# Kernel tuning notes

Hardware: AMD Instinct MI355X
Metric: run time of the kernel (lower is better)

## Reference

```python
import jax, jax.numpy as jnp
import numpy as np

N_NODES = 50000
N_EDGES = 800000
N_LABEL_EDGES = 200000
IN_CH = 256
HID = 64
OUT_CH = 64


def gcn_conv(x, W, b, edge_index, n_nodes):
    """PyG GCNConv: symmetric-normalized aggregation with self-loops.
    out[col] = sum_row norm(row,col) * (x @ W)[row] + b
    """
    xw = x @ W  # [N, out]
    loops = jnp.arange(n_nodes, dtype=edge_index.dtype)
    row = jnp.concatenate([edge_index[0], loops])  # source
    col = jnp.concatenate([edge_index[1], loops])  # target
    deg = jax.ops.segment_sum(jnp.ones_like(col, dtype=xw.dtype), col, num_segments=n_nodes)
    dis = jnp.where(deg > 0, jax.lax.rsqrt(deg), 0.0)
    norm = dis[row] * dis[col]  # [E+N]
    out = jax.ops.segment_sum(xw[row] * norm[:, None], col, num_segments=n_nodes)
    return out + b


def setup_inputs() -> dict:
    key = jax.random.key(0)
    k0, k1, k2, k3, k4 = jax.random.split(key, 5)
    x = jax.random.normal(k0, (N_NODES, IN_CH), dtype=jnp.float32)
    edge_index = jax.random.randint(k1, (2, N_EDGES), 0, N_NODES, dtype=jnp.int32)
    edge_label_index = jax.random.randint(k2, (2, N_LABEL_EDGES), 0, N_NODES, dtype=jnp.int32)
    W1 = jax.random.normal(k3, (IN_CH, HID), dtype=jnp.float32) * (1.0 / np.sqrt(IN_CH))
    b1 = jnp.zeros((HID,), dtype=jnp.float32)
    W2 = jax.random.normal(k4, (HID, OUT_CH), dtype=jnp.float32) * (1.0 / np.sqrt(HID))
    b2 = jnp.zeros((OUT_CH,), dtype=jnp.float32)
    return {"x": x, "edge_index": edge_index, "edge_label_index": edge_label_index,
            "W1": W1, "b1": b1, "W2": W2, "b2": b2}


def reference(x, edge_index, edge_label_index, W1, b1, W2, b2):
    n = x.shape[0]
    # encode: two GCNConv layers with ReLU between
    h = jax.nn.relu(gcn_conv(x, W1, b1, edge_index, n))
    z = gcn_conv(h, W2, b2, edge_index, n)
    # decode: gather node pairs, elementwise multiply, sum over features
    src, dst = edge_label_index[0], edge_label_index[1]
    return jnp.sum(z[src] * z[dst], axis=1)  # [N_LABEL_EDGES]
```

## Files before the change

### kernel.cpp

```cpp
#include <hip/hip_runtime.h>
#include <hip/hip_bf16.h>


constexpr int NC = 512;
constexpr int NBPAD = 256;
constexpr int BSHIFT = 8;

using short8 = __attribute__((ext_vector_type(8))) short;
using f32x4 = __attribute__((ext_vector_type(4))) float;

__device__ __forceinline__ unsigned short f2bf(float f) {
    unsigned u = __float_as_uint(f);
    return (unsigned short)((u + 0x7FFF + ((u >> 16) & 1)) >> 16);
}
__device__ __forceinline__ float bf2f(unsigned short h) {
    return __uint_as_float(((unsigned)h) << 16);
}
__device__ __forceinline__ float4 bf4_to_f4(ushort4 u) {
    return make_float4(bf2f(u.x), bf2f(u.y), bf2f(u.z), bf2f(u.w));
}

__global__ __launch_bounds__(256) void pack_kernel(const float* __restrict__ W1,
                                                   const float* __restrict__ W2,
                                                   unsigned short* __restrict__ Wp1,
                                                   unsigned short* __restrict__ Wp2,
                                                   int* __restrict__ bsums) {
    const int t = threadIdx.x, b = blockIdx.x;
    if (b == 0) {
        bsums[t] = 0;
    } else if (b <= 64) {
        const int idx = (b - 1) * 256 + t;
        const int k = idx >> 6, c = idx & 63;
        Wp1[((k >> 3) * 64 + c) * 8 + (k & 7)] = f2bf(W1[idx]);
    } else {
        const int idx = (b - 65) * 256 + t;
        const int k = idx >> 6, c = idx & 63;
        Wp2[((k >> 3) * 64 + c) * 8 + (k & 7)] = f2bf(W2[idx]);
    }
}

__global__ __launch_bounds__(256) void hist_kernel(const int* __restrict__ col,
                                                   int* __restrict__ histBM,
                                                   int* __restrict__ bsums, int E, int CE) {
    __shared__ int hl[NBPAD];
    const int t = threadIdx.x, c = blockIdx.x;
    hl[t] = 0;
    __syncthreads();
    const int s = c * CE, e = min(E, s + CE);
    for (int i = s + t; i < e; i += 256) atomicAdd(&hl[col[i] >> BSHIFT], 1);
    __syncthreads();
    const int v = hl[t];
    histBM[t * NC + c] = v;
    if (v) atomicAdd(&bsums[t], v);
}

__global__ __launch_bounds__(256) void rowscan_kernel(const int* __restrict__ histBM,
                                                      const int* __restrict__ bsums,
                                                      int* __restrict__ offsBM) {
    __shared__ int red[256];
    __shared__ int sc[256];
    const int t = threadIdx.x, b = blockIdx.x;
    red[t] = (t < b) ? bsums[t] : 0;
    __syncthreads();
    for (int off = 128; off > 0; off >>= 1) {
        if (t < off) red[t] += red[t + off];
        __syncthreads();
    }
    const int base = red[0];
    const int2 a = *(const int2*)&histBM[b * NC + 2 * t];
    const int a0 = a.x, a1 = a.y;
    const int ps = a0 + a1;
    sc[t] = ps;
    __syncthreads();
    for (int off = 1; off < 256; off <<= 1) {
        int u = (t >= off) ? sc[t - off] : 0;
        __syncthreads();
        sc[t] += u;
        __syncthreads();
    }
    const int excl = sc[t] - ps;
    offsBM[b * NC + 2 * t] = base + excl;
    offsBM[b * NC + 2 * t + 1] = base + excl + a0;
}

__global__ __launch_bounds__(256) void reorder_kernel(const int* __restrict__ row,
                                                      const int* __restrict__ col,
                                                      const int* __restrict__ offsBM,
                                                      int* __restrict__ part, int E, int CE) {
    __shared__ int cur[NBPAD];
    const int t = threadIdx.x, c = blockIdx.x;
    cur[t] = offsBM[t * NC + c];
    __syncthreads();
    const int s = c * CE, e = min(E, s + CE);
    for (int i = s + t; i < e; i += 256) {
        const int r = row[i], cl = col[i];
        const int p = atomicAdd(&cur[cl >> BSHIFT], 1);
        part[p] = (r << 8) | (cl & 255);
    }
}

__global__ __launch_bounds__(1024) void bucket_csr_kernel(const int* __restrict__ part,
                                                          const int* __restrict__ offsBM,
                                                          int* __restrict__ csr,
                                                          int* __restrict__ offs,
                                                          float* __restrict__ dis,
                                                          int N, int E, int nbk) {
    __shared__ int cnt[256];
    __shared__ int sc[256];
    const int t = threadIdx.x, b = blockIdx.x;
    const int base = b << BSHIFT;
    const int bstart = offsBM[b * NC];
    const int bend = (b + 1 < NBPAD) ? offsBM[(b + 1) * NC] : E;
    const int m = bend - bstart;
    if (t < 256) cnt[t] = 0;
    __syncthreads();
    for (int i = t; i < m; i += 1024) atomicAdd(&cnt[part[bstart + i] & 255], 1);
    __syncthreads();
    int v = 0;
    if (t < 256) { v = cnt[t]; sc[t] = v; }
    __syncthreads();
    for (int off = 1; off < 256; off <<= 1) {
        int u = 0;
        if (t >= off && t < 256) u = sc[t - off];
        __syncthreads();
        if (t < 256) sc[t] += u;
        __syncthreads();
    }
    if (t < 256) {
        const int excl = sc[t] - v;
        const int node = base + t;
        if (node < N) {
            offs[node] = bstart + excl;
            dis[node] = rsqrtf((float)(v + 1));
        }
        sc[t] = excl;
    }
    __syncthreads();
    for (int i = t; i < m; i += 1024) {
        const int pc = part[bstart + i];
        const int p = atomicAdd(&sc[pc & 255], 1);
        csr[bstart + p] = pc >> 8;
    }
    if (b == nbk - 1 && t == 0) offs[N] = E;
}

template <int K>
__global__ __launch_bounds__(256) void gemm_mfma(const float* __restrict__ X,
                                                 const unsigned short* __restrict__ Wp,
                                                 const float* __restrict__ rowscale,
                                                 unsigned short* __restrict__ Y, int nrows) {
    const int tid = threadIdx.x;
    const int wv = tid >> 6;
    const int lane = tid & 63;
    const int m = lane & 15;
    const int quad = lane >> 4;
    const int rowbase = blockIdx.x * 64 + wv * 16;

    int grow = rowbase + m;
    if (grow >= nrows) grow = nrows - 1;
    const float* xrow = X + (long)grow * K + quad * 8;

    f32x4 acc0 = {0.f, 0.f, 0.f, 0.f};
    f32x4 acc1 = acc0, acc2 = acc0, acc3 = acc0;

    #pragma unroll
    for (int ks = 0; ks < K / 32; ++ks) {
        const float4 a0 = *(const float4*)(xrow + ks * 32);
        const float4 a1 = *(const float4*)(xrow + ks * 32 + 4);
        short8 af;
        af[0] = (short)f2bf(a0.x); af[1] = (short)f2bf(a0.y);
        af[2] = (short)f2bf(a0.z); af[3] = (short)f2bf(a0.w);
        af[4] = (short)f2bf(a1.x); af[5] = (short)f2bf(a1.y);
        af[6] = (short)f2bf(a1.z); af[7] = (short)f2bf(a1.w);
        const unsigned short* bp = Wp + (size_t)((ks * 4 + quad) * 64) * 8;
        const short8 b0 = *(const short8*)(bp + (0 * 16 + m) * 8);
        const short8 b1 = *(const short8*)(bp + (1 * 16 + m) * 8);
        const short8 b2 = *(const short8*)(bp + (2 * 16 + m) * 8);
        const short8 b3 = *(const short8*)(bp + (3 * 16 + m) * 8);
        acc0 = __builtin_amdgcn_mfma_f32_16x16x32_bf16(af, b0, acc0, 0, 0, 0);
        acc1 = __builtin_amdgcn_mfma_f32_16x16x32_bf16(af, b1, acc1, 0, 0, 0);
        acc2 = __builtin_amdgcn_mfma_f32_16x16x32_bf16(af, b2, acc2, 0, 0, 0);
        acc3 = __builtin_amdgcn_mfma_f32_16x16x32_bf16(af, b3, acc3, 0, 0, 0);
    }

    #pragma unroll
    for (int reg = 0; reg < 4; ++reg) {
        const int orow = rowbase + quad * 4 + reg;
        if (orow < nrows) {
            const float d = rowscale[orow];
            unsigned short* yp = Y + (size_t)orow * 64 + m;
            yp[0]  = f2bf(d * acc0[reg]);
            yp[16] = f2bf(d * acc1[reg]);
            yp[32] = f2bf(d * acc2[reg]);
            yp[48] = f2bf(d * acc3[reg]);
        }
    }
}

__device__ __forceinline__ void acc8(float* a, short8 v) {
    #pragma unroll
    for (int j = 0; j < 8; ++j) a[j] += bf2f((unsigned short)v[j]);
}

__global__ __launch_bounds__(256) void agg_gemm_fused(const unsigned short* __restrict__ xs,
                                                      const int* __restrict__ csr,
                                                      const int* __restrict__ offs,
                                                      const float* __restrict__ dis,
                                                      const float* __restrict__ b1,
                                                      const unsigned short* __restrict__ Wp2,
                                                      unsigned short* __restrict__ Y, int n) {
    const int tid = threadIdx.x;
    const int wv = tid >> 6;
    const int lane = tid & 63;
    const int m = lane & 15;
    const int q = lane >> 4;
    const int rowbase = blockIdx.x * 64 + wv * 16;

    int i = rowbase + m;
    if (i >= n) i = n - 1;
    const int off_lo = q * 8;

    float alo[8], ahi[8];
    {
        const unsigned short* xrow = xs + (size_t)i * 64;
        const short8 s0 = *(const short8*)(xrow + off_lo);
        const short8 s1 = *(const short8*)(xrow + 32 + off_lo);
        #pragma unroll
        for (int j = 0; j < 8; ++j) { alo[j] = bf2f((unsigned short)s0[j]); ahi[j] = bf2f((unsigned short)s1[j]); }
    }

    const int s = offs[i];
    const int e = offs[i + 1];
    int j = s;
    int r0 = 0, r1 = 0, r2 = 0, r3 = 0;
    if (j + 3 < e) { r0 = csr[j]; r1 = csr[j + 1]; r2 = csr[j + 2]; r3 = csr[j + 3]; }
    while (j + 3 < e) {
        const int jn = j + 4;
        const int c0 = min(jn,     e - 1), c1 = min(jn + 1, e - 1);
        const int c2 = min(jn + 2, e - 1), c3 = min(jn + 3, e - 1);
        const int n0 = csr[c0], n1 = csr[c1], n2 = csr[c2], n3 = csr[c3];
        const short8 v0l = *(const short8*)(xs + (size_t)r0 * 64 + off_lo);
        const short8 v0h = *(const short8*)(xs + (size_t)r0 * 64 + 32 + off_lo);
        const short8 v1l = *(const short8*)(xs + (size_t)r1 * 64 + off_lo);
        const short8 v1h = *(const short8*)(xs + (size_t)r1 * 64 + 32 + off_lo);
        const short8 v2l = *(const short8*)(xs + (size_t)r2 * 64 + off_lo);
        const short8 v2h = *(const short8*)(xs + (size_t)r2 * 64 + 32 + off_lo);
        const short8 v3l = *(const short8*)(xs + (size_t)r3 * 64 + off_lo);
        const short8 v3h = *(const short8*)(xs + (size_t)r3 * 64 + 32 + off_lo);
        acc8(alo, v0l); acc8(ahi, v0h);
        acc8(alo, v1l); acc8(ahi, v1h);
        acc8(alo, v2l); acc8(ahi, v2h);
        acc8(alo, v3l); acc8(ahi, v3h);
        r0 = n0; r1 = n1; r2 = n2; r3 = n3;
        j = jn;
    }
    for (; j < e; ++j) {
        const int r = csr[j];
        const short8 vl = *(const short8*)(xs + (size_t)r * 64 + off_lo);
        const short8 vh = *(const short8*)(xs + (size_t)r * 64 + 32 + off_lo);
        acc8(alo, vl); acc8(ahi, vh);
    }

    const float di = dis[i];
    float bl[8], bh[8];
    *(float4*)&bl[0] = *(const float4*)(b1 + off_lo);
    *(float4*)&bl[4] = *(const float4*)(b1 + off_lo + 4);
    *(float4*)&bh[0] = *(const float4*)(b1 + 32 + off_lo);
    *(float4*)&bh[4] = *(const float4*)(b1 + 32 + off_lo + 4);
    short8 ha, hb;
    #pragma unroll
    for (int jj = 0; jj < 8; ++jj) {
        ha[jj] = (short)f2bf(fmaxf(fmaf(alo[jj], di, bl[jj]), 0.f));
        hb[jj] = (short)f2bf(fmaxf(fmaf(ahi[jj], di, bh[jj]), 0.f));
    }

    const unsigned short* bplo = Wp2 + (size_t)(q * 64) * 8;
    const unsigned short* bphi = Wp2 + (size_t)((4 + q) * 64) * 8;
    f32x4 c0 = {0.f, 0.f, 0.f, 0.f};
    f32x4 c1 = c0, c2 = c0, c3 = c0;
    const short8 w0l = *(const short8*)(bplo + (0 * 16 + m) * 8);
    const short8 w1l = *(const short8*)(bplo + (1 * 16 + m) * 8);
    const short8 w2l = *(const short8*)(bplo + (2 * 16 + m) * 8);
    const short8 w3l = *(const short8*)(bplo + (3 * 16 + m) * 8);
    const short8 w0h = *(const short8*)(bphi + (0 * 16 + m) * 8);
    const short8 w1h = *(const short8*)(bphi + (1 * 16 + m) * 8);
    const short8 w2h = *(const short8*)(bphi + (2 * 16 + m) * 8);
    const short8 w3h = *(const short8*)(bphi + (3 * 16 + m) * 8);
    c0 = __builtin_amdgcn_mfma_f32_16x16x32_bf16(ha, w0l, c0, 0, 0, 0);
    c0 = __builtin_amdgcn_mfma_f32_16x16x32_bf16(hb, w0h, c0, 0, 0, 0);
    c1 = __builtin_amdgcn_mfma_f32_16x16x32_bf16(ha, w1l, c1, 0, 0, 0);
    c1 = __builtin_amdgcn_mfma_f32_16x16x32_bf16(hb, w1h, c1, 0, 0, 0);
    c2 = __builtin_amdgcn_mfma_f32_16x16x32_bf16(ha, w2l, c2, 0, 0, 0);
    c2 = __builtin_amdgcn_mfma_f32_16x16x32_bf16(hb, w2h, c2, 0, 0, 0);
    c3 = __builtin_amdgcn_mfma_f32_16x16x32_bf16(ha, w3l, c3, 0, 0, 0);
    c3 = __builtin_amdgcn_mfma_f32_16x16x32_bf16(hb, w3h, c3, 0, 0, 0);

    #pragma unroll
    for (int reg = 0; reg < 4; ++reg) {
        const int orow = rowbase + q * 4 + reg;
        if (orow < n) {
            const float d2 = dis[orow];
            unsigned short* yp = Y + (size_t)orow * 64 + m;
            yp[0]  = f2bf(d2 * c0[reg]);
            yp[16] = f2bf(d2 * c1[reg]);
            yp[32] = f2bf(d2 * c2[reg]);
            yp[48] = f2bf(d2 * c3[reg]);
        }
    }
}

__global__ __launch_bounds__(256) void agg_wave(const unsigned short* __restrict__ xs,
                                                const int* __restrict__ csr,
                                                const int* __restrict__ offs,
                                                const float* __restrict__ dis,
                                                const float* __restrict__ bias,
                                                unsigned short* __restrict__ Y, int n) {
    const int tid = threadIdx.x;
    const int wv = tid >> 6;
    const int lane = tid & 63;
    const int m = lane & 15;
    const int q = lane >> 4;
    const int rowbase = blockIdx.x * 64 + wv * 16;

    int i = rowbase + m;
    if (i >= n) i = n - 1;
    const int off_lo = q * 8;

    float alo[8], ahi[8];
    {
        const unsigned short* xrow = xs + (size_t)i * 64;
        const short8 s0 = *(const short8*)(xrow + off_lo);
        const short8 s1 = *(const short8*)(xrow + 32 + off_lo);
        #pragma unroll
        for (int j = 0; j < 8; ++j) { alo[j] = bf2f((unsigned short)s0[j]); ahi[j] = bf2f((unsigned short)s1[j]); }
    }

    const int s = offs[i];
    const int e = offs[i + 1];
    int j = s;
    int r0 = 0, r1 = 0, r2 = 0, r3 = 0;
    if (j + 3 < e) { r0 = csr[j]; r1 = csr[j + 1]; r2 = csr[j + 2]; r3 = csr[j + 3]; }
    while (j + 3 < e) {
        const int jn = j + 4;
        const int c0 = min(jn,     e - 1), c1 = min(jn + 1, e - 1);
        const int c2 = min(jn + 2, e - 1), c3 = min(jn + 3, e - 1);
        const int n0 = csr[c0], n1 = csr[c1], n2 = csr[c2], n3 = csr[c3];
        const short8 v0l = *(const short8*)(xs + (size_t)r0 * 64 + off_lo);
        const short8 v0h = *(const short8*)(xs + (size_t)r0 * 64 + 32 + off_lo);
        const short8 v1l = *(const short8*)(xs + (size_t)r1 * 64 + off_lo);
        const short8 v1h = *(const short8*)(xs + (size_t)r1 * 64 + 32 + off_lo);
        const short8 v2l = *(const short8*)(xs + (size_t)r2 * 64 + off_lo);
        const short8 v2h = *(const short8*)(xs + (size_t)r2 * 64 + 32 + off_lo);
        const short8 v3l = *(const short8*)(xs + (size_t)r3 * 64 + off_lo);
        const short8 v3h = *(const short8*)(xs + (size_t)r3 * 64 + 32 + off_lo);
        acc8(alo, v0l); acc8(ahi, v0h);
        acc8(alo, v1l); acc8(ahi, v1h);
        acc8(alo, v2l); acc8(ahi, v2h);
        acc8(alo, v3l); acc8(ahi, v3h);
        r0 = n0; r1 = n1; r2 = n2; r3 = n3;
        j = jn;
    }
    for (; j < e; ++j) {
        const int r = csr[j];
        const short8 vl = *(const short8*)(xs + (size_t)r * 64 + off_lo);
        const short8 vh = *(const short8*)(xs + (size_t)r * 64 + 32 + off_lo);
        acc8(alo, vl); acc8(ahi, vh);
    }

    const float di = dis[i];
    float bl[8], bh[8];
    *(float4*)&bl[0] = *(const float4*)(bias + off_lo);
    *(float4*)&bl[4] = *(const float4*)(bias + off_lo + 4);
    *(float4*)&bh[0] = *(const float4*)(bias + 32 + off_lo);
    *(float4*)&bh[4] = *(const float4*)(bias + 32 + off_lo + 4);
    short8 ol, oh;
    #pragma unroll
    for (int jj = 0; jj < 8; ++jj) {
        ol[jj] = (short)f2bf(fmaf(alo[jj], di, bl[jj]));
        oh[jj] = (short)f2bf(fmaf(ahi[jj], di, bh[jj]));
    }
    *(short8*)(Y + (size_t)i * 64 + off_lo) = ol;
    *(short8*)(Y + (size_t)i * 64 + 32 + off_lo) = oh;
}

__global__ __launch_bounds__(256) void decode_kernel(const unsigned short* __restrict__ z,
                                                     const int* __restrict__ src,
                                                     const int* __restrict__ dst,
                                                     float* __restrict__ out, int L) {
    const int t = blockIdx.x * 256 + threadIdx.x;
    const int e = t >> 3;
    const int fl = t & 7;
    if (e >= L) return;
    const int s = src[e];
    const int d = dst[e];
    const short8 a = *(const short8*)&z[(long)s * 64 + fl * 8];
    const short8 b = *(const short8*)&z[(long)d * 64 + fl * 8];
    float p = 0.f;
    #pragma unroll
    for (int j = 0; j < 8; ++j)
        p = fmaf(bf2f((unsigned short)a[j]), bf2f((unsigned short)b[j]), p);
    p += __shfl_xor(p, 4); p += __shfl_xor(p, 2); p += __shfl_xor(p, 1);
    if (fl == 0) out[e] = p;
}

extern "C" void kernel_launch(void* const* d_in, const int* in_sizes, int n_in,
                              void* d_out, int out_size, void* d_ws, size_t ws_size,
                              hipStream_t stream) {
    const float* x   = (const float*)d_in[0];
    const int*   ei  = (const int*)d_in[1];
    const int*   eli = (const int*)d_in[2];
    const float* W1  = (const float*)d_in[3];
    const float* b1  = (const float*)d_in[4];
    const float* W2  = (const float*)d_in[5];
    const float* b2  = (const float*)d_in[6];
    float* out = (float*)d_out;

    const int N = in_sizes[0] / 256;
    const int E = in_sizes[1] / 2;
    const int L = in_sizes[2] / 2;
    const int* row = ei;
    const int* col = ei + E;
    const int* src = eli;
    const int* dst = eli + L;

    char* w = (char*)d_ws;
    unsigned short* xs1 = (unsigned short*)w;  w += (size_t)N * 64 * 2;
    unsigned short* xs2 = (unsigned short*)w;  w += (size_t)N * 64 * 2;
    unsigned short* z = (unsigned short*)w;  w += (size_t)N * 64 * 2;
    int*   csr = (int*)w;    w += (size_t)E * 4;
    int*   offs = (int*)w;   w += (size_t)(N + 1) * 4;
    float* dis = (float*)w;  w += (size_t)N * 4;
    int*   part = (int*)w;   w += (size_t)E * 4;
    int* histBM = (int*)w;   w += (size_t)NBPAD * NC * 4;
    int* offsBM = (int*)w;   w += (size_t)NBPAD * NC * 4;
    int* bsums  = (int*)w;   w += NBPAD * 4;
    unsigned short* Wp1 = (unsigned short*)w;  w += (size_t)256 * 64 * 2;
    unsigned short* Wp2 = (unsigned short*)w;  w += (size_t)64 * 64 * 2;

    const int CE = (E + NC - 1) / NC;
    const int nbk = (N + (1 << BSHIFT) - 1) >> BSHIFT;

    pack_kernel<<<81, 256, 0, stream>>>(W1, W2, Wp1, Wp2, bsums);
    hist_kernel<<<NC, 256, 0, stream>>>(col, histBM, bsums, E, CE);
    rowscan_kernel<<<NBPAD, 256, 0, stream>>>(histBM, bsums, offsBM);
    reorder_kernel<<<NC, 256, 0, stream>>>(row, col, offsBM, part, E, CE);
    bucket_csr_kernel<<<nbk, 1024, 0, stream>>>(part, offsBM, csr, offs, dis, N, E, nbk);

    gemm_mfma<256><<<(N + 63) / 64, 256, 0, stream>>>(x, Wp1, dis, xs1, N);
    agg_gemm_fused<<<(N + 63) / 64, 256, 0, stream>>>(xs1, csr, offs, dis, b1, Wp2, xs2, N);
    agg_wave<<<(N + 63) / 64, 256, 0, stream>>>(xs2, csr, offs, dis, b2, z, N);
    decode_kernel<<<(L * 8 + 255) / 256, 256, 0, stream>>>(z, src, dst, out, L);
}
```

Before: 201.0 us.

## Sort nodes by in-degree so aggregation waves process balanced rows

After: 441.5 us. +119.7%, slower.

```diff
diff --git a/kernel.cpp b/kernel.cpp
--- a/kernel.cpp
+++ b/kernel.cpp
@@ -15,19 +15,18 @@
 }
 __device__ __forceinline__ float bf2f(unsigned short h) {
     return __uint_as_float(((unsigned)h) << 16);
-}
-__device__ __forceinline__ float4 bf4_to_f4(ushort4 u) {
-    return make_float4(bf2f(u.x), bf2f(u.y), bf2f(u.z), bf2f(u.w));
 }
 
 __global__ __launch_bounds__(256) void pack_kernel(const float* __restrict__ W1,
                                                    const float* __restrict__ W2,
                                                    unsigned short* __restrict__ Wp1,
                                                    unsigned short* __restrict__ Wp2,
-                                                   int* __restrict__ bsums) {
+                                                   int* __restrict__ bsums,
+                                                   int* __restrict__ dhist) {
     const int t = threadIdx.x, b = blockIdx.x;
     if (b == 0) {
         bsums[t] = 0;
+        dhist[t] = 0;
     } else if (b <= 64) {
         const int idx = (b - 1) * 256 + t;
         const int k = idx >> 6, c = idx & 63;
@@ -104,6 +103,8 @@
                                                           int* __restrict__ csr,
                                                           int* __restrict__ offs,
                                                           float* __restrict__ dis,
+                                                          int* __restrict__ deg,
+                                                          int* __restrict__ dhist,
                                                           int N, int E, int nbk) {
     __shared__ int cnt[256];
     __shared__ int sc[256];
@@ -132,6 +133,8 @@
         if (node < N) {
             offs[node] = bstart + excl;
             dis[node] = rsqrtf((float)(v + 1));
+            deg[node] = v;
+            atomicAdd(&dhist[min(v, 255)], 1);
         }
         sc[t] = excl;
     }
@@ -142,6 +145,31 @@
         csr[bstart + p] = pc >> 8;
     }
     if (b == nbk - 1 && t == 0) offs[N] = E;
+}
+
+__global__ __launch_bounds__(256) void dscan_kernel(const int* __restrict__ dhist,
+                                                    int* __restrict__ dcur) {
+    __shared__ int sc[256];
+    const int t = threadIdx.x;
+    sc[t] = dhist[t];
+    __syncthreads();
+    for (int off = 1; off < 256; off <<= 1) {
+        int u = (t >= off) ? sc[t - off] : 0;
+        __syncthreads();
+        sc[t] += u;
+        __syncthreads();
+    }
+    dcur[t] = sc[255] - sc[t];
+}
+
+__global__ __launch_bounds__(256) void dscatter_kernel(const int* __restrict__ deg,
+                                                       int* __restrict__ dcur,
+                                                       int* __restrict__ perm, int N) {
+    const int node = blockIdx.x * 256 + threadIdx.x;
+    if (node < N) {
+        const int p = atomicAdd(&dcur[min(deg[node], 255)], 1);
+        perm[p] = node;
+    }
 }
 
 template <int K>
@@ -208,6 +236,7 @@
                                                       const float* __restrict__ dis,
                                                       const float* __restrict__ b1,
                                                       const unsigned short* __restrict__ Wp2,
+                                                      const int* __restrict__ perm,
                                                       unsigned short* __restrict__ Y, int n) {
     const int tid = threadIdx.x;
     const int wv = tid >> 6;
@@ -216,8 +245,9 @@
     const int q = lane >> 4;
     const int rowbase = blockIdx.x * 64 + wv * 16;
 
-    int i = rowbase + m;
-    if (i >= n) i = n - 1;
+    int slot = rowbase + m;
+    if (slot >= n) slot = n - 1;
+    const int i = perm[slot];
     const int off_lo = q * 8;
 
     float alo[8], ahi[8];
@@ -297,8 +327,9 @@
 
     #pragma unroll
     for (int reg = 0; reg < 4; ++reg) {
-        const int orow = rowbase + q * 4 + reg;
-        if (orow < n) {
+        const int oslot = rowbase + q * 4 + reg;
+        if (oslot < n) {
+            const int orow = perm[oslot];
             const float d2 = dis[orow];
             unsigned short* yp = Y + (size_t)orow * 64 + m;
             yp[0]  = f2bf(d2 * c0[reg]);
@@ -314,6 +345,7 @@
                                                 const int* __restrict__ offs,
                                                 const float* __restrict__ dis,
                                                 const float* __restrict__ bias,
+                                                const int* __restrict__ perm,
                                                 unsigned short* __restrict__ Y, int n) {
     const int tid = threadIdx.x;
     const int wv = tid >> 6;
@@ -322,8 +354,9 @@
     const int q = lane >> 4;
     const int rowbase = blockIdx.x * 64 + wv * 16;
 
-    int i = rowbase + m;
-    if (i >= n) i = n - 1;
+    int slot = rowbase + m;
+    if (slot >= n) slot = n - 1;
+    const int i = perm[slot];
     const int off_lo = q * 8;
 
     float alo[8], ahi[8];
@@ -436,18 +469,24 @@
     int* bsums  = (int*)w;   w += NBPAD * 4;
     unsigned short* Wp1 = (unsigned short*)w;  w += (size_t)256 * 64 * 2;
     unsigned short* Wp2 = (unsigned short*)w;  w += (size_t)64 * 64 * 2;
+    int* deg   = (int*)w;    w += (size_t)N * 4;
+    int* dhist = (int*)w;    w += 256 * 4;
+    int* dcur  = (int*)w;    w += 256 * 4;
+    int* perm  = (int*)w;    w += (size_t)N * 4;
 
     const int CE = (E + NC - 1) / NC;
     const int nbk = (N + (1 << BSHIFT) - 1) >> BSHIFT;
 
-    pack_kernel<<<81, 256, 0, stream>>>(W1, W2, Wp1, Wp2, bsums);
+    pack_kernel<<<81, 256, 0, stream>>>(W1, W2, Wp1, Wp2, bsums, dhist);
     hist_kernel<<<NC, 256, 0, stream>>>(col, histBM, bsums, E, CE);
     rowscan_kernel<<<NBPAD, 256, 0, stream>>>(histBM, bsums, offsBM);
     reorder_kernel<<<NC, 256, 0, stream>>>(row, col, offsBM, part, E, CE);
-    bucket_csr_kernel<<<nbk, 1024, 0, stream>>>(part, offsBM, csr, offs, dis, N, E, nbk);
+    bucket_csr_kernel<<<nbk, 1024, 0, stream>>>(part, offsBM, csr, offs, dis, deg, dhist, N, E, nbk);
+    dscan_kernel<<<1, 256, 0, stream>>>(dhist, dcur);
+    dscatter_kernel<<<(N + 255) / 256, 256, 0, stream>>>(deg, dcur, perm, N);
 
     gemm_mfma<256><<<(N + 63) / 64, 256, 0, stream>>>(x, Wp1, dis, xs1, N);
-    agg_gemm_fused<<<(N + 63) / 64, 256, 0, stream>>>(xs1, csr, offs, dis, b1, Wp2, xs2, N);
-    agg_wave<<<(N + 63) / 64, 256, 0, stream>>>(xs2, csr, offs, dis, b2, z, N);
+    agg_gemm_fused<<<(N + 63) / 64, 256, 0, stream>>>(xs1, csr, offs, dis, b1, Wp2, perm, xs2, N);
+    agg_wave<<<(N + 63) / 64, 256, 0, stream>>>(xs2, csr, offs, dis, b2, perm, z, N);
     decode_kernel<<<(L * 8 + 255) / 256, 256, 0, stream>>>(z, src, dst, out, L);
 }
```

## Split feature halves across waves in aggregation kernels and unroll gather by eight

Applied to the files above, without the earlier changes.

After: 213.6 us. +6.3%, slower.

```diff
diff --git a/kernel.cpp b/kernel.cpp
--- a/kernel.cpp
+++ b/kernel.cpp
@@ -15,9 +15,6 @@
 }
 __device__ __forceinline__ float bf2f(unsigned short h) {
     return __uint_as_float(((unsigned)h) << 16);
-}
-__device__ __forceinline__ float4 bf4_to_f4(ushort4 u) {
-    return make_float4(bf2f(u.x), bf2f(u.y), bf2f(u.z), bf2f(u.w));
 }
 
 __global__ __launch_bounds__(256) void pack_kernel(const float* __restrict__ W1,
@@ -202,109 +199,117 @@
     for (int j = 0; j < 8; ++j) a[j] += bf2f((unsigned short)v[j]);
 }
 
-__global__ __launch_bounds__(256) void agg_gemm_fused(const unsigned short* __restrict__ xs,
+__device__ __forceinline__ void agg_edges(const unsigned short* __restrict__ xs,
+                                          const int* __restrict__ csr,
+                                          int s, int e, int off, float* acc) {
+    int j = s;
+    int r0 = 0, r1 = 0, r2 = 0, r3 = 0, r4 = 0, r5 = 0, r6 = 0, r7 = 0;
+    if (j + 7 < e) {
+        r0 = csr[j];     r1 = csr[j + 1]; r2 = csr[j + 2]; r3 = csr[j + 3];
+        r4 = csr[j + 4]; r5 = csr[j + 5]; r6 = csr[j + 6]; r7 = csr[j + 7];
+    }
+    while (j + 7 < e) {
+        const int jn = j + 8;
+        const int em1 = e - 1;
+        const int n0 = csr[min(jn,     em1)], n1 = csr[min(jn + 1, em1)];
+        const int n2 = csr[min(jn + 2, em1)], n3 = csr[min(jn + 3, em1)];
+        const int n4 = csr[min(jn + 4, em1)], n5 = csr[min(jn + 5, em1)];
+        const int n6 = csr[min(jn + 6, em1)], n7 = csr[min(jn + 7, em1)];
+        const short8 v0 = *(const short8*)(xs + (size_t)r0 * 64 + off);
+        const short8 v1 = *(const short8*)(xs + (size_t)r1 * 64 + off);
+        const short8 v2 = *(const short8*)(xs + (size_t)r2 * 64 + off);
+        const short8 v3 = *(const short8*)(xs + (size_t)r3 * 64 + off);
+        const short8 v4 = *(const short8*)(xs + (size_t)r4 * 64 + off);
+        const short8 v5 = *(const short8*)(xs + (size_t)r5 * 64 + off);
+        const short8 v6 = *(const short8*)(xs + (size_t)r6 * 64 + off);
+        const short8 v7 = *(const short8*)(xs + (size_t)r7 * 64 + off);
+        acc8(acc, v0); acc8(acc, v1); acc8(acc, v2); acc8(acc, v3);
+        acc8(acc, v4); acc8(acc, v5); acc8(acc, v6); acc8(acc, v7);
+        r0 = n0; r1 = n1; r2 = n2; r3 = n3;
+        r4 = n4; r5 = n5; r6 = n6; r7 = n7;
+        j = jn;
+    }
+    for (; j < e; ++j) {
+        const int r = csr[j];
+        const short8 v = *(const short8*)(xs + (size_t)r * 64 + off);
+        acc8(acc, v);
+    }
+}
+
+__global__ __launch_bounds__(512) void agg_gemm_fused(const unsigned short* __restrict__ xs,
                                                       const int* __restrict__ csr,
                                                       const int* __restrict__ offs,
                                                       const float* __restrict__ dis,
                                                       const float* __restrict__ b1,
                                                       const unsigned short* __restrict__ Wp2,
                                                       unsigned short* __restrict__ Y, int n) {
+    __shared__ float lbuf[4 * 4 * 4 * 64];
     const int tid = threadIdx.x;
-    const int wv = tid >> 6;
+    const int wp = tid >> 6;
+    const int g = wp >> 1;
+    const int hf = wp & 1;
     const int lane = tid & 63;
     const int m = lane & 15;
     const int q = lane >> 4;
-    const int rowbase = blockIdx.x * 64 + wv * 16;
+    const int rowbase = blockIdx.x * 64 + g * 16;
 
     int i = rowbase + m;
     if (i >= n) i = n - 1;
-    const int off_lo = q * 8;
-
-    float alo[8], ahi[8];
+    const int off = hf * 32 + q * 8;
+
+    float acc[8];
     {
-        const unsigned short* xrow = xs + (size_t)i * 64;
-        const short8 s0 = *(const short8*)(xrow + off_lo);
-        const short8 s1 = *(const short8*)(xrow + 32 + off_lo);
+        const short8 s0 = *(const short8*)(xs + (size_t)i * 64 + off);
         #pragma unroll
-        for (int j = 0; j < 8; ++j) { alo[j] = bf2f((unsigned short)s0[j]); ahi[j] = bf2f((unsigned short)s1[j]); }
-    }
-
-    const int s = offs[i];
-    const int e = offs[i + 1];
-    int j = s;
-    int r0 = 0, r1 = 0, r2 = 0, r3 = 0;
-    if (j + 3 < e) { r0 = csr[j]; r1 = csr[j + 1]; r2 = csr[j + 2]; r3 = csr[j + 3]; }
-    while (j + 3 < e) {
-        const int jn = j + 4;
-        const int c0 = min(jn,     e - 1), c1 = min(jn + 1, e - 1);
-        const int c2 = min(jn + 2, e - 1), c3 = min(jn + 3, e - 1);
-        const int n0 = csr[c0], n1 = csr[c1], n2 = csr[c2], n3 = csr[c3];
-        const short8 v0l = *(const short8*)(xs + (size_t)r0 * 64 + off_lo);
-        const short8 v0h = *(const short8*)(xs + (size_t)r0 * 64 + 32 + off_lo);
-        const short8 v1l = *(const short8*)(xs + (size_t)r1 * 64 + off_lo);
-        const short8 v1h = *(const short8*)(xs + (size_t)r1 * 64 + 32 + off_lo);
-        const short8 v2l = *(const short8*)(xs + (size_t)r2 * 64 + off_lo);
-        const short8 v2h = *(const short8*)(xs + (size_t)r2 * 64 + 32 + off_lo);
-        const short8 v3l = *(const short8*)(xs + (size_t)r3 * 64 + off_lo);
-        const short8 v3h = *(const short8*)(xs + (size_t)r3 * 64 + 32 + off_lo);
-        acc8(alo, v0l); acc8(ahi, v0h);
-        acc8(alo, v1l); acc8(ahi, v1h);
-        acc8(alo, v2l); acc8(ahi, v2h);
-        acc8(alo, v3l); acc8(ahi, v3h);
-        r0 = n0; r1 = n1; r2 = n2; r3 = n3;
-        j = jn;
-    }
-    for (; j < e; ++j) {
-        const int r = csr[j];
-        const short8 vl = *(const short8*)(xs + (size_t)r * 64 + off_lo);
-        const short8 vh = *(const short8*)(xs + (size_t)r * 64 + 32 + off_lo);
-        acc8(alo, vl); acc8(ahi, vh);
-    }
+        for (int j = 0; j < 8; ++j) acc[j] = bf2f((unsigned short)s0[j]);
+    }
+    agg_edges(xs, csr, offs[i], offs[i + 1], off, acc);
 
     const float di = dis[i];
-    float bl[8], bh[8];
-    *(float4*)&bl[0] = *(const float4*)(b1 + off_lo);
-    *(float4*)&bl[4] = *(const float4*)(b1 + off_lo + 4);
-    *(float4*)&bh[0] = *(const float4*)(b1 + 32 + off_lo);
-    *(float4*)&bh[4] = *(const float4*)(b1 + 32 + off_lo + 4);
-    short8 ha, hb;
-    #pragma unroll
-    for (int jj = 0; jj < 8; ++jj) {
-        ha[jj] = (short)f2bf(fmaxf(fmaf(alo[jj], di, bl[jj]), 0.f));
-        hb[jj] = (short)f2bf(fmaxf(fmaf(ahi[jj], di, bh[jj]), 0.f));
-    }
-
-    const unsigned short* bplo = Wp2 + (size_t)(q * 64) * 8;
-    const unsigned short* bphi = Wp2 + (size_t)((4 + q) * 64) * 8;
+    float bl[8];
+    *(float4*)&bl[0] = *(const float4*)(b1 + off);
+    *(float4*)&bl[4] = *(const float4*)(b1 + off + 4);
+    short8 hfrag;
+    #pragma unroll
+    for (int jj = 0; jj < 8; ++jj)
+        hfrag[jj] = (short)f2bf(fmaxf(fmaf(acc[jj], di, bl[jj]), 0.f));
+
+    const unsigned short* bp = Wp2 + (size_t)((hf * 4 + q) * 64) * 8;
+    const short8 w0 = *(const short8*)(bp + (0 * 16 + m) * 8);
+    const short8 w1 = *(const short8*)(bp + (1 * 16 + m) * 8);
+    const short8 w2 = *(const short8*)(bp + (2 * 16 + m) * 8);
+    const short8 w3 = *(const short8*)(bp + (3 * 16 + m) * 8);
     f32x4 c0 = {0.f, 0.f, 0.f, 0.f};
     f32x4 c1 = c0, c2 = c0, c3 = c0;
-    const short8 w0l = *(const short8*)(bplo + (0 * 16 + m) * 8);
-    const short8 w1l = *(const short8*)(bplo + (1 * 16 + m) * 8);
-    const short8 w2l = *(const short8*)(bplo + (2 * 16 + m) * 8);
-    const short8 w3l = *(const short8*)(bplo + (3 * 16 + m) * 8);
-    const short8 w0h = *(const short8*)(bphi + (0 * 16 + m) * 8);
-    const short8 w1h = *(const short8*)(bphi + (1 * 16 + m) * 8);
-    const short8 w2h = *(const short8*)(bphi + (2 * 16 + m) * 8);
-    const short8 w3h = *(const short8*)(bphi + (3 * 16 + m) * 8);
-    c0 = __builtin_amdgcn_mfma_f32_16x16x32_bf16(ha, w0l, c0, 0, 0, 0);
-    c0 = __builtin_amdgcn_mfma_f32_16x16x32_bf16(hb, w0h, c0, 0, 0, 0);
-    c1 = __builtin_amdgcn_mfma_f32_16x16x32_bf16(ha, w1l, c1, 0, 0, 0);
-    c1 = __builtin_amdgcn_mfma_f32_16x16x32_bf16(hb, w1h, c1, 0, 0, 0);
-    c2 = __builtin_amdgcn_mfma_f32_16x16x32_bf16(ha, w2l, c2, 0, 0, 0);
-    c2 = __builtin_amdgcn_mfma_f32_16x16x32_bf16(hb, w2h, c2, 0, 0, 0);
-    c3 = __builtin_amdgcn_mfma_f32_16x16x32_bf16(ha, w3l, c3, 0, 0, 0);
-    c3 = __builtin_amdgcn_mfma_f32_16x16x32_bf16(hb, w3h, c3, 0, 0, 0);
-
-    #pragma unroll
-    for (int reg = 0; reg < 4; ++reg) {
-        const int orow = rowbase + q * 4 + reg;
-        if (orow < n) {
-            const float d2 = dis[orow];
-            unsigned short* yp = Y + (size_t)orow * 64 + m;
-            yp[0]  = f2bf(d2 * c0[reg]);
-            yp[16] = f2bf(d2 * c1[reg]);
-            yp[32] = f2bf(d2 * c2[reg]);
-            yp[48] = f2bf(d2 * c3[reg]);
+    c0 = __builtin_amdgcn_mfma_f32_16x16x32_bf16(hfrag, w0, c0, 0, 0, 0);
+    c1 = __builtin_amdgcn_mfma_f32_16x16x32_bf16(hfrag, w1, c1, 0, 0, 0);
+    c2 = __builtin_amdgcn_mfma_f32_16x16x32_bf16(hfrag, w2, c2, 0, 0, 0);
+    c3 = __builtin_amdgcn_mfma_f32_16x16x32_bf16(hfrag, w3, c3, 0, 0, 0);
+
+    if (hf == 1) {
+        float* lb = lbuf + ((g * 4 + 0) * 4) * 64 + lane;
+        #pragma unroll
+        for (int reg = 0; reg < 4; ++reg) {
+            lb[(0 * 4 + reg) * 64] = c0[reg];
+            lb[(1 * 4 + reg) * 64] = c1[reg];
+            lb[(2 * 4 + reg) * 64] = c2[reg];
+            lb[(3 * 4 + reg) * 64] = c3[reg];
+        }
+    }
+    __syncthreads();
+    if (hf == 0) {
+        const float* lb = lbuf + ((g * 4 + 0) * 4) * 64 + lane;
+        #pragma unroll
+        for (int reg = 0; reg < 4; ++reg) {
+            const int orow = rowbase + q * 4 + reg;
+            if (orow < n) {
+                const float d2 = dis[orow];
+                unsigned short* yp = Y + (size_t)orow * 64 + m;
+                yp[0]  = f2bf(d2 * (c0[reg] + lb[(0 * 4 + reg) * 64]));
+                yp[16] = f2bf(d2 * (c1[reg] + lb[(1 * 4 + reg) * 64]));
+                yp[32] = f2bf(d2 * (c2[reg] + lb[(2 * 4 + reg) * 64]));
+                yp[48] = f2bf(d2 * (c3[reg] + lb[(3 * 4 + reg) * 64]));
+            }
         }
     }
 }
@@ -320,67 +325,30 @@
     const int lane = tid & 63;
     const int m = lane & 15;
     const int q = lane >> 4;
+    const int hf = blockIdx.y;
     const int rowbase = blockIdx.x * 64 + wv * 16;
 
     int i = rowbase + m;
     if (i >= n) i = n - 1;
-    const int off_lo = q * 8;
-
-    float alo[8], ahi[8];
+    const int off = hf * 32 + q * 8;
+
+    float acc[8];
     {
-        const unsigned short* xrow = xs + (size_t)i * 64;
-        const short8 s0 = *(const short8*)(xrow + off_lo);
-        const short8 s1 = *(const short8*)(xrow + 32 + off_lo);
+        const short8 s0 = *(const short8*)(xs + (size_t)i * 64 + off);
         #pragma unroll
-        for (int j = 0; j < 8; ++j) { alo[j] = bf2f((unsigned short)s0[j]); ahi[j] = bf2f((unsigned short)s1[j]); }
-    }
-
-    const int s = offs[i];
-    const int e = offs[i + 1];
-    int j = s;
-    int r0 = 0, r1 = 0, r2 = 0, r3 = 0;
-    if (j + 3 < e) { r0 = csr[j]; r1 = csr[j + 1]; r2 = csr[j + 2]; r3 = csr[j + 3]; }
-    while (j + 3 < e) {
-        const int jn = j + 4;
-        const int c0 = min(jn,     e - 1), c1 = min(jn + 1, e - 1);
-        const int c2 = min(jn + 2, e - 1), c3 = min(jn + 3, e - 1);
-        const int n0 = csr[c0], n1 = csr[c1], n2 = csr[c2], n3 = csr[c3];
-        const short8 v0l = *(const short8*)(xs + (size_t)r0 * 64 + off_lo);
-        const short8 v0h = *(const short8*)(xs + (size_t)r0 * 64 + 32 + off_lo);
-        const short8 v1l = *(const short8*)(xs + (size_t)r1 * 64 + off_lo);
-        const short8 v1h = *(const short8*)(xs + (size_t)r1 * 64 + 32 + off_lo);
-        const short8 v2l = *(const short8*)(xs + (size_t)r2 * 64 + off_lo);
-        const short8 v2h = *(const short8*)(xs + (size_t)r2 * 64 + 32 + off_lo);
-        const short8 v3l = *(const short8*)(xs + (size_t)r3 * 64 + off_lo);
-        const short8 v3h = *(const short8*)(xs + (size_t)r3 * 64 + 32 + off_lo);
-        acc8(alo, v0l); acc8(ahi, v0h);
-        acc8(alo, v1l); acc8(ahi, v1h);
-        acc8(alo, v2l); acc8(ahi, v2h);
-        acc8(alo, v3l); acc8(ahi, v3h);
-        r0 = n0; r1 = n1; r2 = n2; r3 = n3;
-        j = jn;
-    }
-    for (; j < e; ++j) {
-        const int r = csr[j];
-        const short8 vl = *(const short8*)(xs + (size_t)r * 64 + off_lo);
-        const short8 vh = *(const short8*)(xs + (size_t)r * 64 + 32 + off_lo);
-        acc8(alo, vl); acc8(ahi, vh);
-    }
+        for (int j = 0; j < 8; ++j) acc[j] = bf2f((unsigned short)s0[j]);
+    }
+    agg_edges(xs, csr, offs[i], offs[i + 1], off, acc);
 
     const float di = dis[i];
-    float bl[8], bh[8];
-    *(float4*)&bl[0] = *(const float4*)(bias + off_lo);
-    *(float4*)&bl[4] = *(const float4*)(bias + off_lo + 4);
-    *(float4*)&bh[0] = *(const float4*)(bias + 32 + off_lo);
-    *(float4*)&bh[4] = *(const float4*)(bias + 32 + off_lo + 4);
-    short8 ol, oh;
-    #pragma unroll
-    for (int jj = 0; jj < 8; ++jj) {
-        ol[jj] = (short)f2bf(fmaf(alo[jj], di, bl[jj]));
-        oh[jj] = (short)f2bf(fmaf(ahi[jj], di, bh[jj]));
-    }
-    *(short8*)(Y + (size_t)i * 64 + off_lo) = ol;
-    *(short8*)(Y + (size_t)i * 64 + 32 + off_lo) = oh;
+    float bl[8];
+    *(float4*)&bl[0] = *(const float4*)(bias + off);
+    *(float4*)&bl[4] = *(const float4*)(bias + off + 4);
+    short8 o;
+    #pragma unroll
+    for (int jj = 0; jj < 8; ++jj)
+        o[jj] = (short)f2bf(fmaf(acc[jj], di, bl[jj]));
+    *(short8*)(Y + (size_t)i * 64 + off) = o;
 }
 
 __global__ __launch_bounds__(256) void decode_kernel(const unsigned short* __restrict__ z,
@@ -447,7 +415,7 @@
     bucket_csr_kernel<<<nbk, 1024, 0, stream>>>(part, offsBM, csr, offs, dis, N, E, nbk);
 
     gemm_mfma<256><<<(N + 63) / 64, 256, 0, stream>>>(x, Wp1, dis, xs1, N);
-    agg_gemm_fused<<<(N + 63) / 64, 256, 0, stream>>>(xs1, csr, offs, dis, b1, Wp2, xs2, N);
-    agg_wave<<<(N + 63) / 64, 256, 0, stream>>>(xs2, csr, offs, dis, b2, z, N);
+    agg_gemm_fused<<<(N + 63) / 64, 512, 0, stream>>>(xs1, csr, offs, dis, b1, Wp2, xs2, N);
+    agg_wave<<<dim3((N + 63) / 64, 2), 256, 0, stream>>>(xs2, csr, offs, dis, b2, z, N);
     decode_kernel<<<(L * 8 + 255) / 256, 256, 0, stream>>>(z, src, dst, out, L);
 }
```
